# Kernel optimization log

Hardware: AMD Instinct MI355X
Metric: run time of the kernel (lower is better)

The kernel has to match this reference:

```python
import jax, jax.numpy as jnp
import numpy as np
from jax import lax


def _conv(x, w, b, stride, pad):
    y = lax.conv_general_dilated(
        x, w, window_strides=(stride, stride),
        padding=[(pad, pad), (pad, pad)],
        dimension_numbers=('NCHW', 'OIHW', 'NCHW'))
    return y + b[None, :, None, None]


def _maxpool3s2(x):
    return lax.reduce_window(x, -jnp.inf, lax.max,
                             (1, 1, 3, 3), (1, 1, 2, 2), 'VALID')


def setup_inputs() -> dict:
    key = jax.random.key(0)
    ks = jax.random.split(key, 16)
    s = 0.05  # weight scale for numerical sanity
    inp = {
        'x': jax.random.normal(ks[0], (128, 3, 224, 224), jnp.float32),
        'w1': jax.random.normal(ks[1], (64, 3, 3, 3), jnp.float32) * s,
        'b1': jnp.zeros((64,), jnp.float32),
        'w2': jax.random.normal(ks[2], (192, 64, 5, 5), jnp.float32) * s,
        'b2': jnp.zeros((192,), jnp.float32),
        'w3': jax.random.normal(ks[3], (384, 192, 3, 3), jnp.float32) * s,
        'b3': jnp.zeros((384,), jnp.float32),
        'w4': jax.random.normal(ks[4], (256, 384, 3, 3), jnp.float32) * s,
        'b4': jnp.zeros((256,), jnp.float32),
        'w5': jax.random.normal(ks[5], (256, 256, 3, 3), jnp.float32) * s,
        'b5': jnp.zeros((256,), jnp.float32),
        'fc1_w': jax.random.normal(ks[6], (4096, 9216), jnp.float32) * 0.01,
        'fc1_b': jnp.zeros((4096,), jnp.float32),
        'fc2_w': jax.random.normal(ks[7], (4096, 4096), jnp.float32) * 0.01,
        'fc2_b': jnp.zeros((4096,), jnp.float32),
        'fc3_w': jax.random.normal(ks[8], (10, 4096), jnp.float32) * 0.01,
        'fc3_b': jnp.zeros((10,), jnp.float32),
        # uniform(0.1, 0.3) per element, matching random.uniform(0.1, 0.3)
        'unif': jax.random.uniform(ks[9], (128, 10), jnp.float32, 0.1, 0.3),
        # np.random.normal(0, 1) noise
        'noise': jax.random.normal(ks[10], (128, 10), jnp.float32),
    }
    return inp


def _forward(x, w1, b1, w2, b2, w3, b3, w4, b4, w5, b5,
             fc1_w, fc1_b, fc2_w, fc2_b, fc3_w, fc3_b, unif, noise):
    # features
    h = jax.nn.relu(_conv(x, w1, b1, stride=4, pad=2))   # [B,64,57,57]
    h = _maxpool3s2(h)                                   # [B,64,28,28]
    h = jax.nn.relu(_conv(h, w2, b2, stride=1, pad=2))   # [B,192,28,28]
    h = _maxpool3s2(h)                                   # [B,192,13,13]
    h = jax.nn.relu(_conv(h, w3, b3, stride=1, pad=1))   # [B,384,13,13]
    h = jax.nn.relu(_conv(h, w4, b4, stride=1, pad=1))   # [B,256,13,13]
    h = jax.nn.relu(_conv(h, w5, b5, stride=1, pad=1))   # [B,256,13,13]
    h = _maxpool3s2(h)                                   # [B,256,6,6]
    # adaptive avgpool to (6,6) is identity at this spatial size
    h = h.reshape(h.shape[0], 256 * 6 * 6)               # [B,9216]
    # classifier (Dropout = identity in eval mode)
    h = jax.nn.relu(h @ fc1_w.T + fc1_b)                 # [B,4096]
    h = jax.nn.relu(h @ fc2_w.T + fc2_b)                 # [B,4096]
    logits = h @ fc3_w.T + fc3_b                         # [B,10]
    # post: keep argmax entry, replace others with unif*max (detached),
    # add Gaussian noise, softmax
    m = jnp.max(logits, axis=-1, keepdims=True)          # [B,1]
    idx = jnp.argmax(logits, axis=-1, keepdims=True)     # first max, like torch
    onehot = jnp.arange(logits.shape[-1])[None, :] == idx
    filled = jnp.where(onehot, logits, unif * lax.stop_gradient(m))
    return jax.nn.softmax(filled + noise, axis=-1)


def reference(x, w1, b1, w2, b2, w3, b3, w4, b4, w5, b5,
              fc1_w, fc1_b, fc2_w, fc2_b, fc3_w, fc3_b, unif, noise):
    return _forward(x, w1, b1, w2, b2, w3, b3, w4, b4, w5, b5,
                    fc1_w, fc1_b, fc2_w, fc2_b, fc3_w, fc3_b, unif, noise)
```

## Files before the change

### kernel.cpp

```cpp
#include <hip/hip_runtime.h>
#include <math.h>


typedef __attribute__((ext_vector_type(4))) float  f32x4;
typedef __attribute__((ext_vector_type(8))) short  bf16x8;

#define OFF_POOL1    106463232ull
#define OFF_X2H      0ull
#define OFF_X2L      12845056ull
#define OFF_WT2H     25690112ull
#define OFF_WT2L     26304512ull
#define OFF_WT3H     26918912ull
#define OFF_WT3L     28246016ull
#define OFF_WT4H     29573120ull
#define OFF_WT4L     31342592ull
#define OFF_WT5H     33112064ull
#define OFF_WT5L     34291712ull
#define OFF_Y2H      36000000ull
#define OFF_Y2L      74535168ull
#define OFF_X3H      113100000ull
#define OFF_X3L      121406688ull
#define OFF_Y3H      36000000ull
#define OFF_Y3L      52613376ull
#define OFF_Y4H      70000000ull
#define OFF_Y4L      81075584ull
#define OFF_Y5H      93000000ull
#define OFF_Y5L      104075584ull
#define OFF_P3       0ull
#define OFF_FC1      5000000ull
#define OFF_FC2      8000000ull
#define OFF_LOG      11000000ull
#define OFF_PART     40000000ull

__device__ inline void bf16split(float v, unsigned short& h, unsigned short& l) {
  unsigned u = __builtin_bit_cast(unsigned, v);
  unsigned hb = (u + 0x7fffu + ((u >> 16) & 1u)) >> 16;
  h = (unsigned short)hb;
  float hf = __builtin_bit_cast(float, hb << 16);
  float r = v - hf;
  unsigned u2 = __builtin_bit_cast(unsigned, r);
  l = (unsigned short)((u2 + 0x7fffu + ((u2 >> 16) & 1u)) >> 16);
}
__device__ inline void bf16split_fast(float v, unsigned short& h, unsigned short& l) {
  unsigned u = __builtin_bit_cast(unsigned, v);
  h = (unsigned short)(u >> 16);
  float r = v - __builtin_bit_cast(float, u & 0xFFFF0000u);
  unsigned u2 = __builtin_bit_cast(unsigned, r);
  l = (unsigned short)((u2 + 0x7fffu + ((u2 >> 16) & 1u)) >> 16);
}
__device__ inline float bf2f(unsigned short h) {
  return __builtin_bit_cast(float, ((unsigned)h) << 16);
}

__global__ __launch_bounds__(256) void conv1_kernel(
    const float* __restrict__ x, const float* __restrict__ w,
    const float* __restrict__ bias, float* __restrict__ out) {
  const int b = blockIdx.y;
  const int s = blockIdx.x * 256 + threadIdx.x;
  if (s >= 57 * 57) return;
  const int oh = s / 57, ow = s % 57;
  float iv[27];
#pragma unroll
  for (int ci = 0; ci < 3; ++ci)
#pragma unroll
    for (int kh = 0; kh < 3; ++kh)
#pragma unroll
      for (int kw = 0; kw < 3; ++kw) {
        const int ih = oh * 4 - 2 + kh;
        const int iw = ow * 4 - 2 + kw;
        float v = 0.f;
        if (ih >= 0 && ih < 224 && iw >= 0 && iw < 224)
          v = x[(((size_t)b * 3 + ci) * 224 + ih) * 224 + iw];
        iv[ci * 9 + kh * 3 + kw] = v;
      }
  for (int co = 0; co < 64; ++co) {
    float a = bias[co];
#pragma unroll
    for (int p = 0; p < 27; ++p) a = fmaf(w[co * 27 + p], iv[p], a);
    out[((size_t)b * 64 + co) * 3249 + s] = fmaxf(a, 0.f);
  }
}

__global__ void maxpool_kernel(const float* __restrict__ in, float* __restrict__ out,
                               int BC, int H, int W, int OH, int OW) {
  const int total = BC * OH * OW;
  for (int idx = blockIdx.x * blockDim.x + threadIdx.x; idx < total;
       idx += gridDim.x * blockDim.x) {
    const int ow = idx % OW;
    int tmp = idx / OW;
    const int oh = tmp % OH;
    const int bc = tmp / OH;
    const float* p = in + (size_t)bc * H * W + (size_t)(oh * 2) * W + ow * 2;
    float m = -INFINITY;
#pragma unroll
    for (int kh = 0; kh < 3; ++kh)
#pragma unroll
      for (int kw = 0; kw < 3; ++kw) m = fmaxf(m, p[kh * W + kw]);
    out[idx] = m;
  }
}

__global__ __launch_bounds__(256) void x2convert_kernel(
    const float* __restrict__ in, unsigned short* __restrict__ xh,
    unsigned short* __restrict__ xl) {
  const int tid = blockIdx.x * 256 + threadIdx.x;
  if (tid >= 128 * 784) return;
  const int b = tid / 784, s = tid % 784;
  for (int cg = 0; cg < 16; ++cg) {
    unsigned short h[4], l[4];
#pragma unroll
    for (int j = 0; j < 4; ++j) {
      const float v = in[((size_t)b * 64 + cg * 4 + j) * 784 + s];
      bf16split(v, h[j], l[j]);
    }
    const size_t g = ((size_t)b * 784 + s) * 64 + cg * 4;
    *reinterpret_cast<uint2*>(xh + g) =
        make_uint2((unsigned)h[0] | ((unsigned)h[1] << 16),
                   (unsigned)h[2] | ((unsigned)h[3] << 16));
    *reinterpret_cast<uint2*>(xl + g) =
        make_uint2((unsigned)l[0] | ((unsigned)l[1] << 16),
                   (unsigned)l[2] | ((unsigned)l[3] << 16));
  }
}

__global__ void wtrans_hl_kernel(const float* __restrict__ w,
                                 unsigned short* __restrict__ wh,
                                 unsigned short* __restrict__ wl,
                                 int C_in, int P, int C_out) {
  const int total = C_out * P * C_in;
  for (int e = blockIdx.x * blockDim.x + threadIdx.x; e < total;
       e += gridDim.x * blockDim.x) {
    const int ci = e % C_in;
    const int p = (e / C_in) % P;
    const int co = e / (C_in * P);
    const float v = w[((size_t)co * C_in + ci) * P + p];
    unsigned short h, l;
    bf16split(v, h, l);
    wh[e] = h; wl[e] = l;
  }
}

__global__ __launch_bounds__(256, 2) void conv2_mfma_kernel(
    const unsigned short* __restrict__ xh, const unsigned short* __restrict__ xl,
    const unsigned short* __restrict__ wh, const unsigned short* __restrict__ wl,
    const float* __restrict__ bias,
    unsigned short* __restrict__ yh, unsigned short* __restrict__ yl) {
  __shared__ unsigned short xt_h[352 * 40];
  __shared__ unsigned short xt_l[352 * 40];
  const int t = threadIdx.x;
  const int lane = t & 63, wv = t >> 6;
  const int b = blockIdx.x;
  const int rg = blockIdx.y;
  const int cg = blockIdx.z;
  const int fr = lane & 15, fq = lane >> 4;
  const int k0 = fq * 8;

  int bofs[4];
#pragma unroll
  for (int ti = 0; ti < 4; ++ti) {
    const int tile = ti * 4 + wv;
    int n = tile * 16 + fr;
    if (tile > 12 || n > 195) n = 195;
    const int r = n / 28, c = n % 28;
    bofs[ti] = (r * 32 + c) * 40 + k0;
  }

  f32x4 acc[4][4];
#pragma unroll
  for (int i = 0; i < 4; ++i)
#pragma unroll
    for (int j = 0; j < 4; ++j) acc[i][j] = (f32x4){0.f, 0.f, 0.f, 0.f};

  for (int cc = 0; cc < 2; ++cc) {
    __syncthreads();
    for (int e = t; e < 1408; e += 256) {
      const int sp = e >> 2, kg = e & 3;
      const int hr = sp >> 5, hc = sp & 31;
      const int ih = rg * 7 + hr - 2, ic = hc - 2;
      uint4 vh = make_uint4(0, 0, 0, 0), vl = make_uint4(0, 0, 0, 0);
      if (ih >= 0 && ih < 28 && ic >= 0 && ic < 28) {
        const size_t g = ((size_t)b * 784 + ih * 28 + ic) * 64 + cc * 32 + kg * 8;
        vh = *reinterpret_cast<const uint4*>(xh + g);
        vl = *reinterpret_cast<const uint4*>(xl + g);
      }
      *reinterpret_cast<uint4*>(xt_h + sp * 40 + kg * 8) = vh;
      *reinterpret_cast<uint4*>(xt_l + sp * 40 + kg * 8) = vl;
    }
    __syncthreads();
#pragma unroll 5
    for (int p = 0; p < 25; ++p) {
      const int kh = p / 5, kw = p % 5;
      bf16x8 a_h[4], a_l[4];
#pragma unroll
      for (int cot = 0; cot < 4; ++cot) {
        const size_t wg = ((size_t)(cg * 64 + cot * 16 + fr) * 25 + p) * 64 + cc * 32 + k0;
        a_h[cot] = __builtin_bit_cast(bf16x8, *reinterpret_cast<const uint4*>(wh + wg));
        a_l[cot] = __builtin_bit_cast(bf16x8, *reinterpret_cast<const uint4*>(wl + wg));
      }
      const int poff = (kh * 32 + kw) * 40;
#pragma unroll
      for (int ti = 0; ti < 4; ++ti) {
        if (ti * 4 + wv <= 12) {
          const bf16x8 b_h = __builtin_bit_cast(bf16x8,
              *reinterpret_cast<const uint4*>(xt_h + bofs[ti] + poff));
          const bf16x8 b_l = __builtin_bit_cast(bf16x8,
              *reinterpret_cast<const uint4*>(xt_l + bofs[ti] + poff));
#pragma unroll
          for (int cot = 0; cot < 4; ++cot) {
            acc[ti][cot] = __builtin_amdgcn_mfma_f32_16x16x32_bf16(a_h[cot], b_h, acc[ti][cot], 0, 0, 0);
            acc[ti][cot] = __builtin_amdgcn_mfma_f32_16x16x32_bf16(a_h[cot], b_l, acc[ti][cot], 0, 0, 0);
            acc[ti][cot] = __builtin_amdgcn_mfma_f32_16x16x32_bf16(a_l[cot], b_h, acc[ti][cot], 0, 0, 0);
          }
        }
      }
    }
  }
#pragma unroll
  for (int cot = 0; cot < 4; ++cot) {
    const int co = cg * 64 + cot * 16 + fq * 4;
    const float4 bi = *reinterpret_cast<const float4*>(bias + co);
    const float bia[4] = {bi.x, bi.y, bi.z, bi.w};
#pragma unroll
    for (int ti = 0; ti < 4; ++ti) {
      const int tile = ti * 4 + wv;
      if (tile > 12) continue;
      const int n = tile * 16 + fr;
      if (n > 195) continue;
      const int oh = rg * 7 + n / 28, ow = n % 28;
      unsigned short h[4], l[4];
#pragma unroll
      for (int r = 0; r < 4; ++r) {
        const float v = fmaxf(acc[ti][cot][r] + bia[r], 0.f);
        bf16split(v, h[r], l[r]);
      }
      const size_t g = ((size_t)b * 784 + oh * 28 + ow) * 192 + co;
      *reinterpret_cast<uint2*>(yh + g) =
          make_uint2((unsigned)h[0] | ((unsigned)h[1] << 16),
                     (unsigned)h[2] | ((unsigned)h[3] << 16));
      *reinterpret_cast<uint2*>(yl + g) =
          make_uint2((unsigned)l[0] | ((unsigned)l[1] << 16),
                     (unsigned)l[2] | ((unsigned)l[3] << 16));
    }
  }
}

__global__ __launch_bounds__(192) void pool2_hl_kernel(
    const unsigned short* __restrict__ yh, const unsigned short* __restrict__ yl,
    unsigned short* __restrict__ xh, unsigned short* __restrict__ xl) {
  const int b = blockIdx.x, oh = blockIdx.y;
  const int c = threadIdx.x;
  for (int ow = 0; ow < 13; ++ow) {
    float m = -INFINITY;
#pragma unroll
    for (int kh = 0; kh < 3; ++kh)
#pragma unroll
      for (int kw = 0; kw < 3; ++kw) {
        const int s = (oh * 2 + kh) * 28 + (ow * 2 + kw);
        const size_t g = ((size_t)b * 784 + s) * 192 + c;
        m = fmaxf(m, bf2f(yh[g]) + bf2f(yl[g]));
      }
    unsigned short h, l;
    bf16split(m, h, l);
    const size_t gd = ((size_t)b * 169 + oh * 13 + ow) * 192 + c;
    xh[gd] = h; xl[gd] = l;
  }
}

__global__ __launch_bounds__(256, 4) void conv13_mfma_kernel(
    const unsigned short* __restrict__ xh, const unsigned short* __restrict__ xl,
    const unsigned short* __restrict__ wh, const unsigned short* __restrict__ wl,
    const float* __restrict__ bias,
    unsigned short* __restrict__ yh, unsigned short* __restrict__ yl,
    int C_in, int C_out) {
  __shared__ unsigned short xt_h[225 * 40];
  __shared__ unsigned short xt_l[225 * 40];
  const int t = threadIdx.x;
  const int lane = t & 63;
  const int wv = t >> 6;
  const int b = blockIdx.x;
  const int co0 = blockIdx.y * 64 + wv * 16;
  const int fr = lane & 15;
  const int fq = lane >> 4;
  const int k0 = fq * 8;

  int bofs[11];
#pragma unroll
  for (int nt = 0; nt < 11; ++nt) {
    int n = nt * 16 + fr;
    if (n > 168) n = 168;
    const int oh = n / 13, ow = n % 13;
    bofs[nt] = (oh * 15 + ow) * 40 + k0;
  }

  f32x4 acc[11];
#pragma unroll
  for (int nt = 0; nt < 11; ++nt) acc[nt] = (f32x4){0.f, 0.f, 0.f, 0.f};

  const int nchunk = C_in >> 5;
  for (int cc = 0; cc < nchunk; ++cc) {
    __syncthreads();
    for (int e = t; e < 900; e += 256) {
      const int sp = e >> 2, kg = e & 3;
      const int r = sp / 15, c = sp % 15;
      const int ir = r - 1, ic = c - 1;
      uint4 vh = make_uint4(0, 0, 0, 0), vl = make_uint4(0, 0, 0, 0);
      if (ir >= 0 && ir < 13 && ic >= 0 && ic < 13) {
        const size_t g = ((size_t)b * 169 + ir * 13 + ic) * C_in + cc * 32 + kg * 8;
        vh = *reinterpret_cast<const uint4*>(xh + g);
        vl = *reinterpret_cast<const uint4*>(xl + g);
      }
      *reinterpret_cast<uint4*>(xt_h + sp * 40 + kg * 8) = vh;
      *reinterpret_cast<uint4*>(xt_l + sp * 40 + kg * 8) = vl;
    }
    __syncthreads();
#pragma unroll
    for (int p = 0; p < 9; ++p) {
      const int kh = p / 3, kw = p % 3;
      const size_t wg = ((size_t)(co0 + fr) * 9 + p) * C_in + cc * 32 + k0;
      const bf16x8 a_h = __builtin_bit_cast(bf16x8, *reinterpret_cast<const uint4*>(wh + wg));
      const bf16x8 a_l = __builtin_bit_cast(bf16x8, *reinterpret_cast<const uint4*>(wl + wg));
      const int poff = (kh * 15 + kw) * 40;
#pragma unroll
      for (int nt = 0; nt < 11; ++nt) {
        const bf16x8 b_h = __builtin_bit_cast(bf16x8,
            *reinterpret_cast<const uint4*>(xt_h + bofs[nt] + poff));
        const bf16x8 b_l = __builtin_bit_cast(bf16x8,
            *reinterpret_cast<const uint4*>(xt_l + bofs[nt] + poff));
        acc[nt] = __builtin_amdgcn_mfma_f32_16x16x32_bf16(a_h, b_h, acc[nt], 0, 0, 0);
        acc[nt] = __builtin_amdgcn_mfma_f32_16x16x32_bf16(a_h, b_l, acc[nt], 0, 0, 0);
        acc[nt] = __builtin_amdgcn_mfma_f32_16x16x32_bf16(a_l, b_h, acc[nt], 0, 0, 0);
      }
    }
  }
  const int co_w = co0 + fq * 4;
  const float4 bi = *reinterpret_cast<const float4*>(bias + co_w);
  const float bia[4] = {bi.x, bi.y, bi.z, bi.w};
#pragma unroll
  for (int nt = 0; nt < 11; ++nt) {
    const int n = nt * 16 + fr;
    if (n > 168) continue;
    unsigned short h[4], l[4];
#pragma unroll
    for (int r = 0; r < 4; ++r) {
      float v = fmaxf(acc[nt][r] + bia[r], 0.f);
      bf16split(v, h[r], l[r]);
    }
    const size_t g = ((size_t)b * 169 + n) * C_out + co_w;
    *reinterpret_cast<uint2*>(yh + g) =
        make_uint2((unsigned)h[0] | ((unsigned)h[1] << 16),
                   (unsigned)h[2] | ((unsigned)h[3] << 16));
    *reinterpret_cast<uint2*>(yl + g) =
        make_uint2((unsigned)l[0] | ((unsigned)l[1] << 16),
                   (unsigned)l[2] | ((unsigned)l[3] << 16));
  }
}

__global__ __launch_bounds__(256) void pool3_hl_kernel(
    const unsigned short* __restrict__ yh, const unsigned short* __restrict__ yl,
    float* __restrict__ out) {
  const int b = blockIdx.x;
  const int s2 = blockIdx.y;
  const int c = threadIdx.x;
  const int oh = s2 / 6, ow = s2 % 6;
  float m = -INFINITY;
#pragma unroll
  for (int kh = 0; kh < 3; ++kh)
#pragma unroll
    for (int kw = 0; kw < 3; ++kw) {
      const int si = (oh * 2 + kh) * 13 + (ow * 2 + kw);
      const size_t g = ((size_t)b * 169 + si) * 256 + c;
      m = fmaxf(m, bf2f(yh[g]) + bf2f(yl[g]));
    }
  out[((size_t)b * 256 + c) * 36 + s2] = m;
}

__global__ __launch_bounds__(256, 2) void fc_mfma_kernel(
    const float* __restrict__ act, const float* __restrict__ Wm,
    float* __restrict__ part, int K, int kchunk, int Cout) {
  __shared__ unsigned short ah[128 * 40];
  __shared__ unsigned short al[128 * 40];
  const int t = threadIdx.x;
  const int lane = t & 63, wv = t >> 6;
  const int m0 = blockIdx.x * 128 + wv * 32;
  const int kb = blockIdx.y * kchunk;
  const int fr = lane & 15, fq = lane >> 4;

  f32x4 acc[2][8];
#pragma unroll
  for (int i = 0; i < 2; ++i)
#pragma unroll
    for (int j = 0; j < 8; ++j) acc[i][j] = (f32x4){0.f, 0.f, 0.f, 0.f};

  for (int kc = kb; kc < kb + kchunk; kc += 32) {
    __syncthreads();
#pragma unroll
    for (int i = 0; i < 4; ++i) {
      const int u = t + i * 256;
      const int n = u >> 3, j = u & 7;
      const float4 v = *reinterpret_cast<const float4*>(act + (size_t)n * K + kc + j * 4);
      const float vv[4] = {v.x, v.y, v.z, v.w};
      unsigned short h[4], l[4];
#pragma unroll
      for (int q = 0; q < 4; ++q) bf16split_fast(vv[q], h[q], l[q]);
      *reinterpret_cast<uint2*>(ah + n * 40 + j * 4) =
          make_uint2((unsigned)h[0] | ((unsigned)h[1] << 16),
                     (unsigned)h[2] | ((unsigned)h[3] << 16));
      *reinterpret_cast<uint2*>(al + n * 40 + j * 4) =
          make_uint2((unsigned)l[0] | ((unsigned)l[1] << 16),
                     (unsigned)l[2] | ((unsigned)l[3] << 16));
    }
    __syncthreads();
    bf16x8 a_h[2], a_l[2];
#pragma unroll
    for (int mt = 0; mt < 2; ++mt) {
      const float* wp = Wm + (size_t)(m0 + mt * 16 + fr) * K + kc + fq * 8;
      const float4 w0 = *reinterpret_cast<const float4*>(wp);
      const float4 w1 = *reinterpret_cast<const float4*>(wp + 4);
      const float ws[8] = {w0.x, w0.y, w0.z, w0.w, w1.x, w1.y, w1.z, w1.w};
#pragma unroll
      for (int q = 0; q < 8; ++q) {
        unsigned short h, l;
        bf16split_fast(ws[q], h, l);
        a_h[mt][q] = (short)h;
        a_l[mt][q] = (short)l;
      }
    }
#pragma unroll
    for (int nt = 0; nt < 8; ++nt) {
      const bf16x8 b_h = __builtin_bit_cast(bf16x8,
          *reinterpret_cast<const uint4*>(ah + (nt * 16 + fr) * 40 + fq * 8));
      const bf16x8 b_l = __builtin_bit_cast(bf16x8,
          *reinterpret_cast<const uint4*>(al + (nt * 16 + fr) * 40 + fq * 8));
#pragma unroll
      for (int mt = 0; mt < 2; ++mt) {
        acc[mt][nt] = __builtin_amdgcn_mfma_f32_16x16x32_bf16(a_h[mt], b_h, acc[mt][nt], 0, 0, 0);
        acc[mt][nt] = __builtin_amdgcn_mfma_f32_16x16x32_bf16(a_h[mt], b_l, acc[mt][nt], 0, 0, 0);
        acc[mt][nt] = __builtin_amdgcn_mfma_f32_16x16x32_bf16(a_l[mt], b_h, acc[mt][nt], 0, 0, 0);
      }
    }
  }
  const size_t base = (size_t)blockIdx.y * Cout * 128;
#pragma unroll
  for (int mt = 0; mt < 2; ++mt) {
#pragma unroll
    for (int nt = 0; nt < 8; ++nt) {
#pragma unroll
      for (int r = 0; r < 4; ++r) {
        const int m = m0 + mt * 16 + fq * 4 + r;
        const int n = nt * 16 + fr;
        part[base + (size_t)m * 128 + n] = acc[mt][nt][r];
      }
    }
  }
}

__global__ __launch_bounds__(256) void fc_reduce_kernel(
    const float* __restrict__ part, const float* __restrict__ bias,
    float* __restrict__ out, int Cout, int KS, int relu) {
  const int g = blockIdx.x * 256 + threadIdx.x;
  if (g >= Cout * 128) return;
  const int n = g & 127, m = g >> 7;
  float s = 0.f;
  for (int ks = 0; ks < KS; ++ks)
    s += part[(size_t)ks * Cout * 128 + (size_t)m * 128 + n];
  s += bias[m];
  if (relu) s = fmaxf(s, 0.f);
  out[(size_t)n * Cout + m] = s;
}

__global__ __launch_bounds__(256) void fc3_kernel(
    const float* __restrict__ A, const float* __restrict__ W,
    const float* __restrict__ bias, float* __restrict__ out) {
  __shared__ float red[256];
  const int b = blockIdx.x;
  const int t = threadIdx.x;
  float acc[10];
#pragma unroll
  for (int n = 0; n < 10; ++n) acc[n] = 0.f;
  const float* a = A + (size_t)b * 4096;
  for (int k = t; k < 4096; k += 256) {
    const float av = a[k];
#pragma unroll
    for (int n = 0; n < 10; ++n) acc[n] = fmaf(av, W[n * 4096 + k], acc[n]);
  }
  for (int n = 0; n < 10; ++n) {
    red[t] = acc[n];
    __syncthreads();
    for (int off = 128; off > 0; off >>= 1) {
      if (t < off) red[t] += red[t + off];
      __syncthreads();
    }
    if (t == 0) out[b * 10 + n] = red[0] + bias[n];
    __syncthreads();
  }
}

__global__ void post_kernel(const float* __restrict__ logits,
                            const float* __restrict__ unif,
                            const float* __restrict__ noise,
                            float* __restrict__ out) {
  const int b = blockIdx.x * blockDim.x + threadIdx.x;
  if (b >= 128) return;
  float lg[10];
#pragma unroll
  for (int j = 0; j < 10; ++j) lg[j] = logits[b * 10 + j];
  float m = lg[0];
  int idx = 0;
#pragma unroll
  for (int j = 1; j < 10; ++j) {
    if (lg[j] > m) { m = lg[j]; idx = j; }
  }
  float v[10];
#pragma unroll
  for (int j = 0; j < 10; ++j)
    v[j] = ((j == idx) ? lg[j] : unif[b * 10 + j] * m) + noise[b * 10 + j];
  float mx = v[0];
#pragma unroll
  for (int j = 1; j < 10; ++j) mx = fmaxf(mx, v[j]);
  float sum = 0.f;
#pragma unroll
  for (int j = 0; j < 10; ++j) { v[j] = expf(v[j] - mx); sum += v[j]; }
  const float inv = 1.f / sum;
#pragma unroll
  for (int j = 0; j < 10; ++j) out[b * 10 + j] = v[j] * inv;
}

extern "C" void kernel_launch(void* const* d_in, const int* in_sizes, int n_in,
                              void* d_out, int out_size, void* d_ws, size_t ws_size,
                              hipStream_t stream) {
  const float* x     = (const float*)d_in[0];
  const float* w1    = (const float*)d_in[1];
  const float* b1    = (const float*)d_in[2];
  const float* w2    = (const float*)d_in[3];
  const float* b2    = (const float*)d_in[4];
  const float* w3    = (const float*)d_in[5];
  const float* b3    = (const float*)d_in[6];
  const float* w4    = (const float*)d_in[7];
  const float* b4    = (const float*)d_in[8];
  const float* w5    = (const float*)d_in[9];
  const float* b5    = (const float*)d_in[10];
  const float* fc1_w = (const float*)d_in[11];
  const float* fc1_b = (const float*)d_in[12];
  const float* fc2_w = (const float*)d_in[13];
  const float* fc2_b = (const float*)d_in[14];
  const float* fc3_w = (const float*)d_in[15];
  const float* fc3_b = (const float*)d_in[16];
  const float* unif  = (const float*)d_in[17];
  const float* noise = (const float*)d_in[18];
  float* out = (float*)d_out;

  char* W = (char*)d_ws;
#define FP(off) ((float*)(W + (off)))
#define US(off) ((unsigned short*)(W + (off)))

  conv1_kernel<<<dim3(13, 128), 256, 0, stream>>>(x, w1, b1, FP(0));
  maxpool_kernel<<<2048, 256, 0, stream>>>(FP(0), FP(OFF_POOL1), 128 * 64, 57, 57, 28, 28);
  x2convert_kernel<<<392, 256, 0, stream>>>(FP(OFF_POOL1), US(OFF_X2H), US(OFF_X2L));
  wtrans_hl_kernel<<<512, 256, 0, stream>>>(w2, US(OFF_WT2H), US(OFF_WT2L), 64, 25, 192);
  wtrans_hl_kernel<<<512, 256, 0, stream>>>(w3, US(OFF_WT3H), US(OFF_WT3L), 192, 9, 384);
  wtrans_hl_kernel<<<512, 256, 0, stream>>>(w4, US(OFF_WT4H), US(OFF_WT4L), 384, 9, 256);
  wtrans_hl_kernel<<<512, 256, 0, stream>>>(w5, US(OFF_WT5H), US(OFF_WT5L), 256, 9, 256);
  conv2_mfma_kernel<<<dim3(128, 4, 3), 256, 0, stream>>>(
      US(OFF_X2H), US(OFF_X2L), US(OFF_WT2H), US(OFF_WT2L), b2,
      US(OFF_Y2H), US(OFF_Y2L));
  pool2_hl_kernel<<<dim3(128, 13), 192, 0, stream>>>(
      US(OFF_Y2H), US(OFF_Y2L), US(OFF_X3H), US(OFF_X3L));
  conv13_mfma_kernel<<<dim3(128, 6), 256, 0, stream>>>(
      US(OFF_X3H), US(OFF_X3L), US(OFF_WT3H), US(OFF_WT3L), b3,
      US(OFF_Y3H), US(OFF_Y3L), 192, 384);
  conv13_mfma_kernel<<<dim3(128, 4), 256, 0, stream>>>(
      US(OFF_Y3H), US(OFF_Y3L), US(OFF_WT4H), US(OFF_WT4L), b4,
      US(OFF_Y4H), US(OFF_Y4L), 384, 256);
  conv13_mfma_kernel<<<dim3(128, 4), 256, 0, stream>>>(
      US(OFF_Y4H), US(OFF_Y4L), US(OFF_WT5H), US(OFF_WT5L), b5,
      US(OFF_Y5H), US(OFF_Y5L), 256, 256);
  pool3_hl_kernel<<<dim3(128, 36), 256, 0, stream>>>(US(OFF_Y5H), US(OFF_Y5L), FP(OFF_P3));
  fc_mfma_kernel<<<dim3(32, 16), 256, 0, stream>>>(FP(OFF_P3), fc1_w, FP(OFF_PART), 9216, 576, 4096);
  fc_reduce_kernel<<<2048, 256, 0, stream>>>(FP(OFF_PART), fc1_b, FP(OFF_FC1), 4096, 16, 1);
  fc_mfma_kernel<<<dim3(32, 16), 256, 0, stream>>>(FP(OFF_FC1), fc2_w, FP(OFF_PART), 4096, 256, 4096);
  fc_reduce_kernel<<<2048, 256, 0, stream>>>(FP(OFF_PART), fc2_b, FP(OFF_FC2), 4096, 16, 1);
  fc3_kernel<<<128, 256, 0, stream>>>(FP(OFF_FC2), fc3_w, fc3_b, FP(OFF_LOG));
  post_kernel<<<1, 128, 0, stream>>>(FP(OFF_LOG), unif, noise, out);
}
```

Measured before the change: 894.5 us.

## Fuse maxpool1 into bf16 split, prefetch weights and group MFMAs in convs

The standalone first maxpool is folded into the bf16 hi/lo convert kernel, so conv1's output is pooled directly while converting. This removes one kernel launch and a full float round trip of the pooled tensor, and conv1's output buffer moves to a workspace offset reused later by the weight-transpose outputs. The conv2 and conv3-5 MFMA loops now load the next filter tap's weights one iteration ahead. In those loops and the FC GEMM, all LDS operand loads are issued before MFMAs are grouped by split term, to hide load latency and spread out dependent accumulator chains. The cost is more live registers, which could reduce occupancy.

Measured after the change: 874.3 us. 2.3% less time.

```diff
diff --git a/kernel.cpp b/kernel.cpp
--- a/kernel.cpp
+++ b/kernel.cpp
@@ -5,7 +5,7 @@
 typedef __attribute__((ext_vector_type(4))) float  f32x4;
 typedef __attribute__((ext_vector_type(8))) short  bf16x8;
 
-#define OFF_POOL1    106463232ull
+#define OFF_C1O      25690112ull
 #define OFF_X2H      0ull
 #define OFF_X2L      12845056ull
 #define OFF_WT2H     25690112ull
@@ -81,37 +81,25 @@
   }
 }
 
-__global__ void maxpool_kernel(const float* __restrict__ in, float* __restrict__ out,
-                               int BC, int H, int W, int OH, int OW) {
-  const int total = BC * OH * OW;
-  for (int idx = blockIdx.x * blockDim.x + threadIdx.x; idx < total;
-       idx += gridDim.x * blockDim.x) {
-    const int ow = idx % OW;
-    int tmp = idx / OW;
-    const int oh = tmp % OH;
-    const int bc = tmp / OH;
-    const float* p = in + (size_t)bc * H * W + (size_t)(oh * 2) * W + ow * 2;
-    float m = -INFINITY;
-#pragma unroll
-    for (int kh = 0; kh < 3; ++kh)
-#pragma unroll
-      for (int kw = 0; kw < 3; ++kw) m = fmaxf(m, p[kh * W + kw]);
-    out[idx] = m;
-  }
-}
-
-__global__ __launch_bounds__(256) void x2convert_kernel(
+__global__ __launch_bounds__(256) void pool1cvt_kernel(
     const float* __restrict__ in, unsigned short* __restrict__ xh,
     unsigned short* __restrict__ xl) {
   const int tid = blockIdx.x * 256 + threadIdx.x;
   if (tid >= 128 * 784) return;
   const int b = tid / 784, s = tid % 784;
+  const int oh = s / 28, ow = s % 28;
+  const float* base = in + (size_t)b * 64 * 3249 + (size_t)(oh * 2) * 57 + ow * 2;
   for (int cg = 0; cg < 16; ++cg) {
     unsigned short h[4], l[4];
 #pragma unroll
     for (int j = 0; j < 4; ++j) {
-      const float v = in[((size_t)b * 64 + cg * 4 + j) * 784 + s];
-      bf16split(v, h[j], l[j]);
+      const float* p = base + (size_t)(cg * 4 + j) * 3249;
+      float m = -INFINITY;
+#pragma unroll
+      for (int kh = 0; kh < 3; ++kh)
+#pragma unroll
+        for (int kw = 0; kw < 3; ++kw) m = fmaxf(m, p[kh * 57 + kw]);
+      bf16split(m, h[j], l[j]);
     }
     const size_t g = ((size_t)b * 784 + s) * 64 + cg * 4;
     *reinterpret_cast<uint2*>(xh + g) =
@@ -156,9 +144,11 @@
   const int k0 = fq * 8;
 
   int bofs[4];
+  bool act[4];
 #pragma unroll
   for (int ti = 0; ti < 4; ++ti) {
     const int tile = ti * 4 + wv;
+    act[ti] = (tile <= 12);
     int n = tile * 16 + fr;
     if (tile > 12 || n > 195) n = 195;
     const int r = n / 28, c = n % 28;
@@ -187,31 +177,55 @@
       *reinterpret_cast<uint4*>(xt_l + sp * 40 + kg * 8) = vl;
     }
     __syncthreads();
+
+    bf16x8 cur_h[4], cur_l[4];
+#pragma unroll
+    for (int cot = 0; cot < 4; ++cot) {
+      const size_t wg = ((size_t)(cg * 64 + cot * 16 + fr) * 25) * 64 + cc * 32 + k0;
+      cur_h[cot] = __builtin_bit_cast(bf16x8, *reinterpret_cast<const uint4*>(wh + wg));
+      cur_l[cot] = __builtin_bit_cast(bf16x8, *reinterpret_cast<const uint4*>(wl + wg));
+    }
 #pragma unroll 5
     for (int p = 0; p < 25; ++p) {
+      bf16x8 nxt_h[4], nxt_l[4];
+      if (p < 24) {
+#pragma unroll
+        for (int cot = 0; cot < 4; ++cot) {
+          const size_t wg = ((size_t)(cg * 64 + cot * 16 + fr) * 25 + (p + 1)) * 64 + cc * 32 + k0;
+          nxt_h[cot] = __builtin_bit_cast(bf16x8, *reinterpret_cast<const uint4*>(wh + wg));
+          nxt_l[cot] = __builtin_bit_cast(bf16x8, *reinterpret_cast<const uint4*>(wl + wg));
+        }
+      }
       const int kh = p / 5, kw = p % 5;
-      bf16x8 a_h[4], a_l[4];
-#pragma unroll
-      for (int cot = 0; cot < 4; ++cot) {
-        const size_t wg = ((size_t)(cg * 64 + cot * 16 + fr) * 25 + p) * 64 + cc * 32 + k0;
-        a_h[cot] = __builtin_bit_cast(bf16x8, *reinterpret_cast<const uint4*>(wh + wg));
-        a_l[cot] = __builtin_bit_cast(bf16x8, *reinterpret_cast<const uint4*>(wl + wg));
-      }
       const int poff = (kh * 32 + kw) * 40;
+      bf16x8 bh[4], bl[4];
 #pragma unroll
       for (int ti = 0; ti < 4; ++ti) {
-        if (ti * 4 + wv <= 12) {
-          const bf16x8 b_h = __builtin_bit_cast(bf16x8,
+        if (act[ti]) {
+          bh[ti] = __builtin_bit_cast(bf16x8,
               *reinterpret_cast<const uint4*>(xt_h + bofs[ti] + poff));
-          const bf16x8 b_l = __builtin_bit_cast(bf16x8,
+          bl[ti] = __builtin_bit_cast(bf16x8,
               *reinterpret_cast<const uint4*>(xt_l + bofs[ti] + poff));
-#pragma unroll
-          for (int cot = 0; cot < 4; ++cot) {
-            acc[ti][cot] = __builtin_amdgcn_mfma_f32_16x16x32_bf16(a_h[cot], b_h, acc[ti][cot], 0, 0, 0);
-            acc[ti][cot] = __builtin_amdgcn_mfma_f32_16x16x32_bf16(a_h[cot], b_l, acc[ti][cot], 0, 0, 0);
-            acc[ti][cot] = __builtin_amdgcn_mfma_f32_16x16x32_bf16(a_l[cot], b_h, acc[ti][cot], 0, 0, 0);
-          }
         }
+      }
+#pragma unroll
+      for (int ti = 0; ti < 4; ++ti) if (act[ti])
+#pragma unroll
+        for (int cot = 0; cot < 4; ++cot)
+          acc[ti][cot] = __builtin_amdgcn_mfma_f32_16x16x32_bf16(cur_h[cot], bh[ti], acc[ti][cot], 0, 0, 0);
+#pragma unroll
+      for (int ti = 0; ti < 4; ++ti) if (act[ti])
+#pragma unroll
+        for (int cot = 0; cot < 4; ++cot)
+          acc[ti][cot] = __builtin_amdgcn_mfma_f32_16x16x32_bf16(cur_h[cot], bl[ti], acc[ti][cot], 0, 0, 0);
+#pragma unroll
+      for (int ti = 0; ti < 4; ++ti) if (act[ti])
+#pragma unroll
+        for (int cot = 0; cot < 4; ++cot)
+          acc[ti][cot] = __builtin_amdgcn_mfma_f32_16x16x32_bf16(cur_l[cot], bh[ti], acc[ti][cot], 0, 0, 0);
+      if (p < 24) {
+#pragma unroll
+        for (int cot = 0; cot < 4; ++cot) { cur_h[cot] = nxt_h[cot]; cur_l[cot] = nxt_l[cot]; }
       }
     }
   }
@@ -296,6 +310,7 @@
 #pragma unroll
   for (int nt = 0; nt < 11; ++nt) acc[nt] = (f32x4){0.f, 0.f, 0.f, 0.f};
 
+  const size_t wrow = (size_t)(co0 + fr) * 9;
   const int nchunk = C_in >> 5;
   for (int cc = 0; cc < nchunk; ++cc) {
     __syncthreads();
@@ -313,23 +328,41 @@
       *reinterpret_cast<uint4*>(xt_l + sp * 40 + kg * 8) = vl;
     }
     __syncthreads();
+    const int cbase = cc * 32 + k0;
+    bf16x8 ca_h = __builtin_bit_cast(bf16x8, *reinterpret_cast<const uint4*>(wh + wrow * C_in + cbase));
+    bf16x8 ca_l = __builtin_bit_cast(bf16x8, *reinterpret_cast<const uint4*>(wl + wrow * C_in + cbase));
 #pragma unroll
     for (int p = 0; p < 9; ++p) {
-      const int kh = p / 3, kw = p % 3;
-      const size_t wg = ((size_t)(co0 + fr) * 9 + p) * C_in + cc * 32 + k0;
-      const bf16x8 a_h = __builtin_bit_cast(bf16x8, *reinterpret_cast<const uint4*>(wh + wg));
-      const bf16x8 a_l = __builtin_bit_cast(bf16x8, *reinterpret_cast<const uint4*>(wl + wg));
-      const int poff = (kh * 15 + kw) * 40;
-#pragma unroll
-      for (int nt = 0; nt < 11; ++nt) {
-        const bf16x8 b_h = __builtin_bit_cast(bf16x8,
-            *reinterpret_cast<const uint4*>(xt_h + bofs[nt] + poff));
-        const bf16x8 b_l = __builtin_bit_cast(bf16x8,
-            *reinterpret_cast<const uint4*>(xt_l + bofs[nt] + poff));
-        acc[nt] = __builtin_amdgcn_mfma_f32_16x16x32_bf16(a_h, b_h, acc[nt], 0, 0, 0);
-        acc[nt] = __builtin_amdgcn_mfma_f32_16x16x32_bf16(a_h, b_l, acc[nt], 0, 0, 0);
-        acc[nt] = __builtin_amdgcn_mfma_f32_16x16x32_bf16(a_l, b_h, acc[nt], 0, 0, 0);
-      }
+      bf16x8 na_h, na_l;
+      if (p < 8) {
+        na_h = __builtin_bit_cast(bf16x8, *reinterpret_cast<const uint4*>(wh + (wrow + p + 1) * C_in + cbase));
+        na_l = __builtin_bit_cast(bf16x8, *reinterpret_cast<const uint4*>(wl + (wrow + p + 1) * C_in + cbase));
+      }
+      const int poff = ((p / 3) * 15 + (p % 3)) * 40;
+#pragma unroll
+      for (int q = 0; q < 3; ++q) {
+        const int nq = (q < 2) ? 4 : 3;
+        bf16x8 bh[4], bl[4];
+#pragma unroll
+        for (int i = 0; i < 4; ++i) {
+          if (i < nq) {
+            bh[i] = __builtin_bit_cast(bf16x8,
+                *reinterpret_cast<const uint4*>(xt_h + bofs[q * 4 + i] + poff));
+            bl[i] = __builtin_bit_cast(bf16x8,
+                *reinterpret_cast<const uint4*>(xt_l + bofs[q * 4 + i] + poff));
+          }
+        }
+#pragma unroll
+        for (int i = 0; i < 4; ++i) if (i < nq)
+          acc[q * 4 + i] = __builtin_amdgcn_mfma_f32_16x16x32_bf16(ca_h, bh[i], acc[q * 4 + i], 0, 0, 0);
+#pragma unroll
+        for (int i = 0; i < 4; ++i) if (i < nq)
+          acc[q * 4 + i] = __builtin_amdgcn_mfma_f32_16x16x32_bf16(ca_h, bl[i], acc[q * 4 + i], 0, 0, 0);
+#pragma unroll
+        for (int i = 0; i < 4; ++i) if (i < nq)
+          acc[q * 4 + i] = __builtin_amdgcn_mfma_f32_16x16x32_bf16(ca_l, bh[i], acc[q * 4 + i], 0, 0, 0);
+      }
+      if (p < 8) { ca_h = na_h; ca_l = na_l; }
     }
   }
   const int co_w = co0 + fq * 4;
@@ -426,17 +459,31 @@
       }
     }
 #pragma unroll
-    for (int nt = 0; nt < 8; ++nt) {
-      const bf16x8 b_h = __builtin_bit_cast(bf16x8,
-          *reinterpret_cast<const uint4*>(ah + (nt * 16 + fr) * 40 + fq * 8));
-      const bf16x8 b_l = __builtin_bit_cast(bf16x8,
-          *reinterpret_cast<const uint4*>(al + (nt * 16 + fr) * 40 + fq * 8));
-#pragma unroll
-      for (int mt = 0; mt < 2; ++mt) {
-        acc[mt][nt] = __builtin_amdgcn_mfma_f32_16x16x32_bf16(a_h[mt], b_h, acc[mt][nt], 0, 0, 0);
-        acc[mt][nt] = __builtin_amdgcn_mfma_f32_16x16x32_bf16(a_h[mt], b_l, acc[mt][nt], 0, 0, 0);
-        acc[mt][nt] = __builtin_amdgcn_mfma_f32_16x16x32_bf16(a_l[mt], b_h, acc[mt][nt], 0, 0, 0);
-      }
+    for (int np = 0; np < 4; ++np) {
+      bf16x8 bh[2], bl[2];
+#pragma unroll
+      for (int i = 0; i < 2; ++i) {
+        const int nt = np * 2 + i;
+        bh[i] = __builtin_bit_cast(bf16x8,
+            *reinterpret_cast<const uint4*>(ah + (nt * 16 + fr) * 40 + fq * 8));
+        bl[i] = __builtin_bit_cast(bf16x8,
+            *reinterpret_cast<const uint4*>(al + (nt * 16 + fr) * 40 + fq * 8));
+      }
+#pragma unroll
+      for (int i = 0; i < 2; ++i)
+#pragma unroll
+        for (int mt = 0; mt < 2; ++mt)
+          acc[mt][np * 2 + i] = __builtin_amdgcn_mfma_f32_16x16x32_bf16(a_h[mt], bh[i], acc[mt][np * 2 + i], 0, 0, 0);
+#pragma unroll
+      for (int i = 0; i < 2; ++i)
+#pragma unroll
+        for (int mt = 0; mt < 2; ++mt)
+          acc[mt][np * 2 + i] = __builtin_amdgcn_mfma_f32_16x16x32_bf16(a_h[mt], bl[i], acc[mt][np * 2 + i], 0, 0, 0);
+#pragma unroll
+      for (int i = 0; i < 2; ++i)
+#pragma unroll
+        for (int mt = 0; mt < 2; ++mt)
+          acc[mt][np * 2 + i] = __builtin_amdgcn_mfma_f32_16x16x32_bf16(a_l[mt], bh[i], acc[mt][np * 2 + i], 0, 0, 0);
     }
   }
   const size_t base = (size_t)blockIdx.y * Cout * 128;
@@ -553,9 +600,8 @@
 #define FP(off) ((float*)(W + (off)))
 #define US(off) ((unsigned short*)(W + (off)))
 
-  conv1_kernel<<<dim3(13, 128), 256, 0, stream>>>(x, w1, b1, FP(0));
-  maxpool_kernel<<<2048, 256, 0, stream>>>(FP(0), FP(OFF_POOL1), 128 * 64, 57, 57, 28, 28);
-  x2convert_kernel<<<392, 256, 0, stream>>>(FP(OFF_POOL1), US(OFF_X2H), US(OFF_X2L));
+  conv1_kernel<<<dim3(13, 128), 256, 0, stream>>>(x, w1, b1, FP(OFF_C1O));
+  pool1cvt_kernel<<<392, 256, 0, stream>>>(FP(OFF_C1O), US(OFF_X2H), US(OFF_X2L));
   wtrans_hl_kernel<<<512, 256, 0, stream>>>(w2, US(OFF_WT2H), US(OFF_WT2L), 64, 25, 192);
   wtrans_hl_kernel<<<512, 256, 0, stream>>>(w3, US(OFF_WT3H), US(OFF_WT3L), 192, 9, 384);
   wtrans_hl_kernel<<<512, 256, 0, stream>>>(w4, US(OFF_WT4H), US(OFF_WT4L), 384, 9, 256);
```
